# Performance work log

Hardware: AMD Instinct MI355X
Metric: run time of the kernel (lower is better)

## Reference

```python
import jax, jax.numpy as jnp
import numpy as np

NUM_ENTITIES = 500000
NUM_RELATIONS = 100
DIM = 64
BATCH = 4096
N_MEM = 256


def setup_inputs() -> dict:
    key = jax.random.key(0)
    ks = jax.random.split(key, 12)
    # xavier_uniform bound for [N, D]: sqrt(6/(N+D))
    def xavier(k, shape):
        bound = np.sqrt(6.0 / (shape[0] + shape[1]))
        return jax.random.uniform(k, shape, jnp.float32, -bound, bound)
    inp = {
        "item_ids": jax.random.randint(ks[0], (BATCH,), 0, NUM_ENTITIES),
        "hop0_h": jax.random.randint(ks[1], (BATCH, N_MEM), 0, NUM_ENTITIES),
        "hop0_r": jax.random.randint(ks[2], (BATCH, N_MEM), 0, NUM_RELATIONS),
        "hop0_t": jax.random.randint(ks[3], (BATCH, N_MEM), 0, NUM_ENTITIES),
        "hop1_h": jax.random.randint(ks[4], (BATCH, N_MEM), 0, NUM_ENTITIES),
        "hop1_r": jax.random.randint(ks[5], (BATCH, N_MEM), 0, NUM_RELATIONS),
        "hop1_t": jax.random.randint(ks[6], (BATCH, N_MEM), 0, NUM_ENTITIES),
        "entity_emb": xavier(ks[7], (NUM_ENTITIES, DIM)),
        "relation_emb": xavier(ks[8], (NUM_RELATIONS, DIM)),
        "W0": xavier(ks[9], (DIM, DIM)),  # nn.Linear weight [out, in]
        "W1": xavier(ks[10], (DIM, DIM)),
    }
    return inp


def _hop(item_emb, h_idx, r_idx, t_idx, entity_emb, relation_emb, W):
    h = entity_emb[h_idx]          # [B, M, D]
    r = relation_emb[r_idx]        # [B, M, D]
    t = entity_emb[t_idx]          # [B, M, D]
    hr = h * r
    attn = jax.nn.softmax(jnp.einsum("bmd,bd->bm", hr, item_emb), axis=-1)
    o = jnp.einsum("bm,bmd->bd", attn, t)
    return (item_emb + o) @ W.T    # Linear(bias=False): x @ W^T


def reference(item_ids, hop0_h, hop0_r, hop0_t, hop1_h, hop1_r, hop1_t,
              entity_emb, relation_emb, W0, W1):
    item_emb = entity_emb[item_ids]  # [B, D]
    item_emb = _hop(item_emb, hop0_h, hop0_r, hop0_t, entity_emb, relation_emb, W0)
    item_emb = _hop(item_emb, hop1_h, hop1_r, hop1_t, entity_emb, relation_emb, W1)
    return item_emb.sum(axis=-1)     # [B]
```

## Files before the change

### kernel.cpp

```cpp
#include <hip/hip_runtime.h>

#define NMEM 256
#define DIM  64


__global__ __launch_bounds__(256, 4)
void ripplenet_kernel(const int* __restrict__ item_ids,
                      const int* __restrict__ h0, const int* __restrict__ r0, const int* __restrict__ t0,
                      const int* __restrict__ h1, const int* __restrict__ r1, const int* __restrict__ t1,
                      const float* __restrict__ ent, const float* __restrict__ rel,
                      const float* __restrict__ W0, const float* __restrict__ W1,
                      float* __restrict__ out)
{
    __shared__ float4 sRedO[64];
    __shared__ float4 sRedY[64];
    __shared__ float  sSm[4];

    const int tid  = threadIdx.x;
    const int lane = tid & 63;
    const int wave = tid >> 6;
    const int g    = lane >> 4;
    const int l16  = lane & 15;
    const int b    = blockIdx.x;

    const float4* ent4 = (const float4*)ent;
    const float4* rel4 = (const float4*)rel;

    float4 xv = ent4[item_ids[b] * 16 + l16];

    const int base = b * NMEM + wave * 64 + lane;

    for (int hop = 0; hop < 2; ++hop) {
        const int ih = (hop ? h1 : h0)[base];
        const int ir = (hop ? r1 : r0)[base];
        const int it = (hop ? t1 : t0)[base];
        const float4* W4 = (const float4*)(hop ? W1 : W0);

        float4 acc = {0.f, 0.f, 0.f, 0.f};
        float  sm  = 0.f;

        #pragma unroll 4
        for (int i = 0; i < 16; ++i) {
            int j2  = i * 4 + g;
            int ihj = __shfl(ih, j2, 64);
            int irj = __shfl(ir, j2, 64);
            int itj = __shfl(it, j2, 64);
            float4 hv = ent4[ihj * 16 + l16];
            float4 rv = rel4[irj * 16 + l16];
            float4 tv = ent4[itj * 16 + l16];
            float v = hv.x*rv.x*xv.x + hv.y*rv.y*xv.y + hv.z*rv.z*xv.z + hv.w*rv.w*xv.w;
            v += __shfl_xor(v, 1, 64);
            v += __shfl_xor(v, 2, 64);
            v += __shfl_xor(v, 4, 64);
            v += __shfl_xor(v, 8, 64);
            float p = __expf(v);
            sm    += p;
            acc.x += p * tv.x; acc.y += p * tv.y;
            acc.z += p * tv.z; acc.w += p * tv.w;
        }

        acc.x += __shfl_xor(acc.x, 16, 64); acc.y += __shfl_xor(acc.y, 16, 64);
        acc.z += __shfl_xor(acc.z, 16, 64); acc.w += __shfl_xor(acc.w, 16, 64);
        acc.x += __shfl_xor(acc.x, 32, 64); acc.y += __shfl_xor(acc.y, 32, 64);
        acc.z += __shfl_xor(acc.z, 32, 64); acc.w += __shfl_xor(acc.w, 32, 64);
        sm += __shfl_xor(sm, 16, 64);
        sm += __shfl_xor(sm, 32, 64);

        if (lane < 16) sRedO[wave * 16 + lane] = acc;
        if (lane == 0) sSm[wave] = sm;
        __syncthreads();

        float smt = sSm[0] + sSm[1] + sSm[2] + sSm[3];
        float inv = 1.0f / smt;
        float4 o0 = sRedO[l16],      o1 = sRedO[16 + l16];
        float4 o2 = sRedO[32 + l16], o3 = sRedO[48 + l16];
        float4 xo;
        xo.x = xv.x + (o0.x + o1.x + o2.x + o3.x) * inv;
        xo.y = xv.y + (o0.y + o1.y + o2.y + o3.y) * inv;
        xo.z = xv.z + (o0.z + o1.z + o2.z + o3.z) * inv;
        xo.w = xv.w + (o0.w + o1.w + o2.w + o3.w) * inv;

        int k = wave * 4 + g;
        float xod0 = __shfl(xo.x, k, 64);
        float xod1 = __shfl(xo.y, k, 64);
        float xod2 = __shfl(xo.z, k, 64);
        float xod3 = __shfl(xo.w, k, 64);
        float4 w0 = W4[(l16 * 4 + 0) * 16 + k];
        float4 w1 = W4[(l16 * 4 + 1) * 16 + k];
        float4 w2 = W4[(l16 * 4 + 2) * 16 + k];
        float4 w3 = W4[(l16 * 4 + 3) * 16 + k];
        float4 y;
        y.x = xod0*w0.x + xod1*w0.y + xod2*w0.z + xod3*w0.w;
        y.y = xod0*w1.x + xod1*w1.y + xod2*w1.z + xod3*w1.w;
        y.z = xod0*w2.x + xod1*w2.y + xod2*w2.z + xod3*w2.w;
        y.w = xod0*w3.x + xod1*w3.y + xod2*w3.z + xod3*w3.w;

        y.x += __shfl_xor(y.x, 16, 64); y.y += __shfl_xor(y.y, 16, 64);
        y.z += __shfl_xor(y.z, 16, 64); y.w += __shfl_xor(y.w, 16, 64);
        y.x += __shfl_xor(y.x, 32, 64); y.y += __shfl_xor(y.y, 32, 64);
        y.z += __shfl_xor(y.z, 32, 64); y.w += __shfl_xor(y.w, 32, 64);

        if (lane < 16) sRedY[wave * 16 + lane] = y;
        __syncthreads();

        float4 y0 = sRedY[l16],      y1 = sRedY[16 + l16];
        float4 y2 = sRedY[32 + l16], y3 = sRedY[48 + l16];
        xv.x = y0.x + y1.x + y2.x + y3.x;
        xv.y = y0.y + y1.y + y2.y + y3.y;
        xv.z = y0.z + y1.z + y2.z + y3.z;
        xv.w = y0.w + y1.w + y2.w + y3.w;
    }

    if (wave == 0) {
        float s = xv.x + xv.y + xv.z + xv.w;
        s += __shfl_xor(s, 1, 64);
        s += __shfl_xor(s, 2, 64);
        s += __shfl_xor(s, 4, 64);
        s += __shfl_xor(s, 8, 64);
        if (lane == 0) out[b] = s;
    }
}

extern "C" void kernel_launch(void* const* d_in, const int* in_sizes, int n_in,
                              void* d_out, int out_size, void* d_ws, size_t ws_size,
                              hipStream_t stream) {
    const int*   item_ids = (const int*)  d_in[0];
    const int*   h0       = (const int*)  d_in[1];
    const int*   r0       = (const int*)  d_in[2];
    const int*   t0       = (const int*)  d_in[3];
    const int*   h1       = (const int*)  d_in[4];
    const int*   r1       = (const int*)  d_in[5];
    const int*   t1       = (const int*)  d_in[6];
    const float* ent      = (const float*)d_in[7];
    const float* rel      = (const float*)d_in[8];
    const float* W0       = (const float*)d_in[9];
    const float* W1       = (const float*)d_in[10];
    float* out = (float*)d_out;

    ripplenet_kernel<<<4096, 256, 0, stream>>>(item_ids, h0, r0, t0, h1, r1, t1,
                                               ent, rel, W0, W1, out);
}
```

Baseline: 322.7 us.

## Compute W projection redundantly per wave to drop barrier and prefetch indices

```diff
diff --git a/kernel.cpp b/kernel.cpp
--- a/kernel.cpp
+++ b/kernel.cpp
@@ -12,9 +12,8 @@
                       const float* __restrict__ W0, const float* __restrict__ W1,
                       float* __restrict__ out)
 {
-    __shared__ float4 sRedO[64];
-    __shared__ float4 sRedY[64];
-    __shared__ float  sSm[4];
+    __shared__ float4 sRedO[2][64];
+    __shared__ float  sSm[2][4];
 
     const int tid  = threadIdx.x;
     const int lane = tid & 63;
@@ -26,25 +25,27 @@
     const float4* ent4 = (const float4*)ent;
     const float4* rel4 = (const float4*)rel;
 
+    const int base = b * NMEM + wave * 64 + lane;
+    const int ihA = h0[base], irA = r0[base], itA = t0[base];
+    const int ihB = h1[base], irB = r1[base], itB = t1[base];
+
     float4 xv = ent4[item_ids[b] * 16 + l16];
 
-    const int base = b * NMEM + wave * 64 + lane;
-
     for (int hop = 0; hop < 2; ++hop) {
-        const int ih = (hop ? h1 : h0)[base];
-        const int ir = (hop ? r1 : r0)[base];
-        const int it = (hop ? t1 : t0)[base];
+        const int ih = hop ? ihB : ihA;
+        const int ir = hop ? irB : irA;
+        const int it = hop ? itB : itA;
         const float4* W4 = (const float4*)(hop ? W1 : W0);
 
         float4 acc = {0.f, 0.f, 0.f, 0.f};
         float  sm  = 0.f;
 
-        #pragma unroll 4
+        #pragma unroll
         for (int i = 0; i < 16; ++i) {
-            int j2  = i * 4 + g;
-            int ihj = __shfl(ih, j2, 64);
-            int irj = __shfl(ir, j2, 64);
-            int itj = __shfl(it, j2, 64);
+            int j   = i * 4 + g;
+            int ihj = __shfl(ih, j, 64);
+            int irj = __shfl(ir, j, 64);
+            int itj = __shfl(it, j, 64);
             float4 hv = ent4[ihj * 16 + l16];
             float4 rv = rel4[irj * 16 + l16];
             float4 tv = ent4[itj * 16 + l16];
@@ -66,58 +67,46 @@
         sm += __shfl_xor(sm, 16, 64);
         sm += __shfl_xor(sm, 32, 64);
 
-        if (lane < 16) sRedO[wave * 16 + lane] = acc;
-        if (lane == 0) sSm[wave] = sm;
+        if (lane < 16) sRedO[hop][wave * 16 + lane] = acc;
+        if (lane == 0) sSm[hop][wave] = sm;
         __syncthreads();
 
-        float smt = sSm[0] + sSm[1] + sSm[2] + sSm[3];
+        float smt = sSm[hop][0] + sSm[hop][1] + sSm[hop][2] + sSm[hop][3];
         float inv = 1.0f / smt;
-        float4 o0 = sRedO[l16],      o1 = sRedO[16 + l16];
-        float4 o2 = sRedO[32 + l16], o3 = sRedO[48 + l16];
+        float4 o0 = sRedO[hop][l16],      o1 = sRedO[hop][16 + l16];
+        float4 o2 = sRedO[hop][32 + l16], o3 = sRedO[hop][48 + l16];
         float4 xo;
         xo.x = xv.x + (o0.x + o1.x + o2.x + o3.x) * inv;
         xo.y = xv.y + (o0.y + o1.y + o2.y + o3.y) * inv;
         xo.z = xv.z + (o0.z + o1.z + o2.z + o3.z) * inv;
         xo.w = xv.w + (o0.w + o1.w + o2.w + o3.w) * inv;
 
-        int k = wave * 4 + g;
-        float xod0 = __shfl(xo.x, k, 64);
-        float xod1 = __shfl(xo.y, k, 64);
-        float xod2 = __shfl(xo.z, k, 64);
-        float xod3 = __shfl(xo.w, k, 64);
-        float4 w0 = W4[(l16 * 4 + 0) * 16 + k];
-        float4 w1 = W4[(l16 * 4 + 1) * 16 + k];
-        float4 w2 = W4[(l16 * 4 + 2) * 16 + k];
-        float4 w3 = W4[(l16 * 4 + 3) * 16 + k];
-        float4 y;
-        y.x = xod0*w0.x + xod1*w0.y + xod2*w0.z + xod3*w0.w;
-        y.y = xod0*w1.x + xod1*w1.y + xod2*w1.z + xod3*w1.w;
-        y.z = xod0*w2.x + xod1*w2.y + xod2*w2.z + xod3*w2.w;
-        y.w = xod0*w3.x + xod1*w3.y + xod2*w3.z + xod3*w3.w;
+        float y = 0.f;
+        #pragma unroll
+        for (int k = 0; k < 16; ++k) {
+            float bx = __shfl(xo.x, k, 64);
+            float by = __shfl(xo.y, k, 64);
+            float bz = __shfl(xo.z, k, 64);
+            float bw = __shfl(xo.w, k, 64);
+            float4 w = W4[lane * 16 + k];
+            y += bx*w.x + by*w.y + bz*w.z + bw*w.w;
+        }
 
-        y.x += __shfl_xor(y.x, 16, 64); y.y += __shfl_xor(y.y, 16, 64);
-        y.z += __shfl_xor(y.z, 16, 64); y.w += __shfl_xor(y.w, 16, 64);
-        y.x += __shfl_xor(y.x, 32, 64); y.y += __shfl_xor(y.y, 32, 64);
-        y.z += __shfl_xor(y.z, 32, 64); y.w += __shfl_xor(y.w, 32, 64);
-
-        if (lane < 16) sRedY[wave * 16 + lane] = y;
-        __syncthreads();
-
-        float4 y0 = sRedY[l16],      y1 = sRedY[16 + l16];
-        float4 y2 = sRedY[32 + l16], y3 = sRedY[48 + l16];
-        xv.x = y0.x + y1.x + y2.x + y3.x;
-        xv.y = y0.y + y1.y + y2.y + y3.y;
-        xv.z = y0.z + y1.z + y2.z + y3.z;
-        xv.w = y0.w + y1.w + y2.w + y3.w;
-    }
-
-    if (wave == 0) {
-        float s = xv.x + xv.y + xv.z + xv.w;
-        s += __shfl_xor(s, 1, 64);
-        s += __shfl_xor(s, 2, 64);
-        s += __shfl_xor(s, 4, 64);
-        s += __shfl_xor(s, 8, 64);
-        if (lane == 0) out[b] = s;
+        if (hop == 0) {
+            xv.x = __shfl(y, l16 * 4 + 0, 64);
+            xv.y = __shfl(y, l16 * 4 + 1, 64);
+            xv.z = __shfl(y, l16 * 4 + 2, 64);
+            xv.w = __shfl(y, l16 * 4 + 3, 64);
+        } else if (wave == 0) {
+            float s = y;
+            s += __shfl_xor(s,  1, 64);
+            s += __shfl_xor(s,  2, 64);
+            s += __shfl_xor(s,  4, 64);
+            s += __shfl_xor(s,  8, 64);
+            s += __shfl_xor(s, 16, 64);
+            s += __shfl_xor(s, 32, 64);
+            if (lane == 0) out[b] = s;
+        }
     }
 }
 
```

Result: slower. 342.3 us (+6.1%).
